# Kernel tuning notes

Hardware: AMD Instinct MI355X
Metric: run time of the kernel (lower is better)

## Reference

```python
import jax, jax.numpy as jnp
import numpy as np
import math

# hyperparams matching init_kwargs
GAMMA_S = 0.8
GAMMA_U = 0.8
RHO_I = 0.1
RHO_T = 0.1
EPS = 1e-10
TAU_MIN = 0.005
TAU_MAX = 1.0
TAU_INIT = 0.07
GRAD_CLIP = 5.0
ETA_INIT = 0.01
ETA_MIN = 0.0001
N_STATE = 2900000
BSZ = 4096
DIM = 1024


def setup_inputs() -> dict:
    key = jax.random.key(0)
    k1, k2 = jax.random.split(key)
    imf = jax.random.normal(k1, (BSZ, DIM), jnp.float32)
    imf = imf / jnp.linalg.norm(imf, axis=1, keepdims=True)
    txf = jax.random.normal(k2, (BSZ, DIM), jnp.float32)
    txf = txf / jnp.linalg.norm(txf, axis=1, keepdims=True)
    return {
        "image_features": imf,
        "text_features": txf,
        "s_I": jnp.zeros((N_STATE,), jnp.float32),
        "s_T": jnp.zeros((N_STATE,), jnp.float32),
        "tau_I": jnp.full((N_STATE,), TAU_INIT, jnp.float32),
        "tau_T": jnp.full((N_STATE,), TAU_INIT, jnp.float32),
        "u_I": jnp.zeros((N_STATE,), jnp.float32),
        "u_T": jnp.zeros((N_STATE,), jnp.float32),
        "b_I": jnp.zeros((N_STATE,), jnp.float32),
        "b_T": jnp.zeros((N_STATE,), jnp.float32),
        "image_ids": jnp.arange(BSZ, dtype=jnp.int32),
        "text_ids": jnp.arange(BSZ, dtype=jnp.int32),
        "epoch": 5,
        "max_epoch": 30,
    }


def reference(image_features, text_features, s_I, s_T, tau_I, tau_T,
              u_I, u_T, b_I, b_T, image_ids, text_ids, epoch, max_epoch):
    B = image_features.shape[0]
    sim = jnp.einsum('id,jd->ij', image_features, text_features)  # [B,B]
    diag_sim = jnp.diagonal(sim)                                  # [B]

    tau_image = tau_I[image_ids]  # [B]
    tau_text = tau_T[text_ids]    # [B]

    image_diffs = sim - diag_sim[:, None]
    text_diffs = sim - diag_sim[None, :]
    # .detach() in torch -> stop_gradient
    idt = jax.lax.stop_gradient(image_diffs / tau_image[:, None])
    tdt = jax.lax.stop_gradient(text_diffs / tau_text[None, :])

    # max-trick state b_I / b_T: running row/col max per sample id
    old_b_I = b_I[image_ids]
    new_b_I = jnp.maximum(jnp.max(idt, axis=1), old_b_I)  # [B]
    old_b_T = b_T[text_ids]
    new_b_T = jnp.maximum(jnp.max(tdt, axis=0), old_b_T)  # [B]

    exp_image_diffs = jnp.exp(idt - new_b_I[:, None])
    exp_text_diffs = jnp.exp(tdt - new_b_T[None, :])
    g_I = jnp.sum(exp_image_diffs, axis=1, keepdims=True) / (B - 1)  # [B,1]
    g_T = jnp.sum(exp_text_diffs, axis=0, keepdims=True) / (B - 1)   # [1,B]

    # moving-average s state (compute_last=False, last_g_* = None path)
    s_I_new = (1.0 - GAMMA_S) * s_I[image_ids] * jnp.exp(old_b_I - new_b_I) + GAMMA_S * g_I[:, 0]
    s_T_new = (1.0 - GAMMA_S) * s_T[text_ids] * jnp.exp(old_b_T - new_b_T) + GAMMA_S * g_T[0, :]
    s_I_b = s_I_new[:, None]  # same shape as g_I
    s_T_b = s_T_new[None, :]  # same shape as g_T

    weights_image = exp_image_diffs / (s_I_b + EPS)
    weights_text = exp_text_diffs / (s_T_b + EPS)

    image_loss = jnp.sum(weights_image * image_diffs, axis=1, keepdims=True) / (B - 1)
    text_loss = jnp.sum(weights_text * text_diffs, axis=0, keepdims=True) / (B - 1)
    total_loss = image_loss.mean() + text_loss.mean()

    grad_tau_image = (jnp.log(s_I_b) + new_b_I[:, None] + RHO_I
                      - jnp.sum(weights_image * idt, axis=1, keepdims=True) / (B - 1))
    grad_tau_text = (jnp.log(s_T_b) + new_b_T[None, :] + RHO_T
                     - jnp.sum(weights_text * tdt, axis=0, keepdims=True) / (B - 1))

    u_I_new = (1.0 - GAMMA_U) * u_I[image_ids] + GAMMA_U * jnp.clip(grad_tau_image[:, 0], -GRAD_CLIP, GRAD_CLIP)
    u_T_new = (1.0 - GAMMA_U) * u_T[text_ids] + GAMMA_U * jnp.clip(grad_tau_text[0, :], -GRAD_CLIP, GRAD_CLIP)

    eta_cur = ETA_MIN + (ETA_INIT - ETA_MIN) * math.cos(math.pi * (epoch / max_epoch) / 2)
    tau_I_new = jnp.clip(tau_image - eta_cur * u_I_new, TAU_MIN, TAU_MAX)
    tau_T_new = jnp.clip(tau_text - eta_cur * u_T_new, TAU_MIN, TAU_MAX)

    # scattered state writes (the module's in-place buffer updates)
    b_I_out = b_I.at[image_ids].set(new_b_I)
    b_T_out = b_T.at[text_ids].set(new_b_T)
    s_I_out = s_I.at[image_ids].set(s_I_new)
    s_T_out = s_T.at[text_ids].set(s_T_new)
    u_I_out = u_I.at[image_ids].set(u_I_new)
    u_T_out = u_T.at[text_ids].set(u_T_new)
    tau_I_out = tau_I.at[image_ids].set(tau_I_new)
    tau_T_out = tau_T.at[text_ids].set(tau_T_new)

    avg_image_tau = tau_image.mean()
    avg_text_tau = tau_text.mean()

    return (g_I, g_T, grad_tau_image, grad_tau_text, total_loss,
            avg_image_tau, avg_text_tau,
            s_I_out, s_T_out, u_I_out, u_T_out,
            b_I_out, b_T_out, tau_I_out, tau_T_out)
```

## Files before the change

### kernel.cpp

```cpp
#include <hip/hip_runtime.h>
#include <math.h>

#define BSZ 4096
#define DIM 1024
#define NST 2900000

constexpr float GAMMA_S   = 0.8f;
constexpr float GAMMA_U   = 0.8f;
constexpr float RHO_I_C   = 0.1f;
constexpr float RHO_T_C   = 0.1f;
constexpr float C_EPS     = 1e-10f;
constexpr float TAU_MIN_C = 0.005f;
constexpr float TAU_MAX_C = 1.0f;
constexpr float GCLIP     = 5.0f;
constexpr float ETA_INIT_C = 0.01f;
constexpr float ETA_MIN_C  = 1e-4f;
constexpr float PI_F       = 3.14159265358979323846f;

typedef __bf16 bf16x8 __attribute__((ext_vector_type(8)));
typedef float  f32x4  __attribute__((ext_vector_type(4)));

__device__ __forceinline__ unsigned short f2bf(float f) {
    unsigned int u = __float_as_uint(f);
    u += 0x7fffu + ((u >> 16) & 1u);
    return (unsigned short)(u >> 16);
}
__device__ __forceinline__ float bf2f(unsigned short s) {
    return __uint_as_float(((unsigned int)s) << 16);
}

__global__ __launch_bounds__(256) void conv_diag(const float* __restrict__ imf,
                                                 const float* __restrict__ txf,
                                                 unsigned short* __restrict__ abf,
                                                 unsigned short* __restrict__ bbf,
                                                 const float* __restrict__ tau_I,
                                                 const float* __restrict__ tau_T,
                                                 const float* __restrict__ b_I,
                                                 const float* __restrict__ b_T,
                                                 const int* __restrict__ iid,
                                                 const int* __restrict__ tid_,
                                                 float* diag, float* tauIg, float* tauTg,
                                                 float* obI, float* obT,
                                                 float* __restrict__ scal) {
    if (blockIdx.x == 0 && threadIdx.x < 3) scal[threadIdx.x] = 0.f;
    const int w  = threadIdx.x >> 6;
    const int ln = threadIdx.x & 63;
    const int i  = blockIdx.x * 4 + w;
    float dot = 0.f;
#pragma unroll
    for (int k = 0; k < 4; ++k) {
        const int off = i * DIM + k * 256 + ln * 4;
        float4 a = *(const float4*)&imf[off];
        float4 b = *(const float4*)&txf[off];
        ushort4 ra, rb;
        ra.x = f2bf(a.x); ra.y = f2bf(a.y); ra.z = f2bf(a.z); ra.w = f2bf(a.w);
        rb.x = f2bf(b.x); rb.y = f2bf(b.y); rb.z = f2bf(b.z); rb.w = f2bf(b.w);
        *(ushort4*)&abf[off] = ra;
        *(ushort4*)&bbf[off] = rb;
        dot += bf2f(ra.x) * bf2f(rb.x) + bf2f(ra.y) * bf2f(rb.y) +
               bf2f(ra.z) * bf2f(rb.z) + bf2f(ra.w) * bf2f(rb.w);
    }
#pragma unroll
    for (int m = 32; m; m >>= 1) dot += __shfl_xor(dot, m);
    if (ln == 0) {
        diag[i] = dot;
        const int id = iid[i];
        tauIg[i] = tau_I[id];
        obI[i]   = b_I[id];
        const int td = tid_[i];
        tauTg[i] = tau_T[td];
        obT[i]   = b_T[td];
    }
}

__device__ __forceinline__ void async16(const void* g, void* l) {
    __builtin_amdgcn_global_load_lds(
        (const __attribute__((address_space(1))) void*)g,
        (__attribute__((address_space(3))) void*)l, 16, 0, 0);
}

__global__ __launch_bounds__(256) void gemm_fused(const unsigned short* __restrict__ A,
                                                  const unsigned short* __restrict__ B,
                                                  const float* __restrict__ diag,
                                                  const float* __restrict__ tauIg,
                                                  const float* __restrict__ tauTg,
                                                  float* __restrict__ rpM,
                                                  float* __restrict__ rpE,
                                                  float* __restrict__ rpV,
                                                  float* __restrict__ cpM,
                                                  float* __restrict__ cpE,
                                                  float* __restrict__ cpV,
                                                  const float* __restrict__ s_I,
                                                  const float* __restrict__ s_T,
                                                  const float* __restrict__ u_I,
                                                  const float* __restrict__ u_T,
                                                  const float* __restrict__ b_I,
                                                  const float* __restrict__ b_T,
                                                  const float* __restrict__ tau_I,
                                                  const float* __restrict__ tau_T,
                                                  float* __restrict__ outbase) {
    __shared__ unsigned short As[128 * 64];
    __shared__ unsigned short Bs[128 * 64];

    const int tid = threadIdx.x;
    const int gid = ((blockIdx.x >> 4) << 3) | (blockIdx.x & 7);

    if ((blockIdx.x >> 3) & 1) {
        const size_t idx = (size_t)gid * 256 + tid;
        const size_t stride = (size_t)1024 * 256;
        const size_t NV = (NST - 1) / 4;
        const float* srcs[8] = {s_I, s_T, u_I, u_T, b_I, b_T, tau_I, tau_T};
#pragma unroll
        for (int a = 0; a < 8; ++a) {
            const float* s = srcs[a];
            float* d = outbase + (size_t)a * NST;
            for (size_t cidx = idx; cidx < NV; cidx += stride) {
                const float4 f = *(const float4*)&s[4 * cidx];
                const float nx = s[4 * cidx + 4];
                *(float4*)&d[1 + 4 * cidx] = make_float4(f.y, f.z, f.w, nx);
            }
            if (idx == 0) d[0] = s[0];
            if (idx < 3)  d[NST - 3 + idx] = s[NST - 3 + idx];
        }
        return;
    }

    const int bjIdx = gid & 31, biIdx = gid >> 5;
    const int bi = biIdx * 128;
    const int bj = bjIdx * 128;
    const int lane = tid & 63;
    const int wave = tid >> 6;
    const int m_base = (wave >> 1) * 64;
    const int n_base = (wave & 1) * 64;

    f32x4 acc[4][4];
#pragma unroll
    for (int m = 0; m < 4; ++m)
#pragma unroll
        for (int n = 0; n < 4; ++n)
            acc[m][n] = (f32x4){0.f, 0.f, 0.f, 0.f};

    const int mrow = lane & 15;
    const int q    = lane >> 4;

    for (int k0 = 0; k0 < DIM; k0 += 64) {
        __syncthreads();
#pragma unroll
        for (int j = 0; j < 4; ++j) {
            const int c   = tid + j * 256;
            const int row = c >> 3;
            const int kk  = ((c & 7) ^ (row & 7)) << 3;
            async16(&A[(size_t)(bi + row) * DIM + k0 + kk], &As[c * 8]);
            async16(&B[(size_t)(bj + row) * DIM + k0 + kk], &Bs[c * 8]);
        }
        __syncthreads();
#pragma unroll
        for (int ks = 0; ks < 2; ++ks) {
            bf16x8 af[4], bfr[4];
#pragma unroll
            for (int t = 0; t < 4; ++t) {
                const int rlA = m_base + t * 16 + mrow;
                const int rlB = n_base + t * 16 + mrow;
                const int slA = (((ks << 2) + q) ^ (rlA & 7)) << 3;
                const int slB = (((ks << 2) + q) ^ (rlB & 7)) << 3;
                af[t]  = *(const bf16x8*)&As[rlA * 64 + slA];
                bfr[t] = *(const bf16x8*)&Bs[rlB * 64 + slB];
            }
#pragma unroll
            for (int mt = 0; mt < 4; ++mt)
#pragma unroll
                for (int nt = 0; nt < 4; ++nt)
                    acc[mt][nt] = __builtin_amdgcn_mfma_f32_16x16x32_bf16(
                        af[mt], bfr[nt], acc[mt][nt], 0, 0, 0);
        }
    }

    __syncthreads();
    float* prm = (float*)Bs;
    if (tid < 128) {
        prm[tid]       = diag[bi + tid];
        prm[128 + tid] = 1.0f / tauIg[bi + tid];
        prm[256 + tid] = diag[bj + tid];
        prm[384 + tid] = 1.0f / tauTg[bj + tid];
    }
    __syncthreads();

    float* red = (float*)As;
    const int rowq = (lane >> 4) * 4;

#pragma unroll
    for (int mt = 0; mt < 4; ++mt)
#pragma unroll
        for (int r = 0; r < 4; ++r) {
            const int row_l = m_base + mt * 16 + rowq + r;
            const float dgr = prm[row_l];
            const float itr = prm[128 + row_l];
            float v0 = (acc[mt][0][r] - dgr) * itr;
            float v1 = (acc[mt][1][r] - dgr) * itr;
            float v2 = (acc[mt][2][r] - dgr) * itr;
            float v3 = (acc[mt][3][r] - dgr) * itr;
            float m = fmaxf(fmaxf(v0, v1), fmaxf(v2, v3));
#pragma unroll
            for (int x = 1; x <= 8; x <<= 1) m = fmaxf(m, __shfl_xor(m, x));
            const float e0 = __expf(v0 - m), e1 = __expf(v1 - m);
            const float e2 = __expf(v2 - m), e3 = __expf(v3 - m);
            float se = e0 + e1 + e2 + e3;
            float sv = e0 * v0 + e1 * v1 + e2 * v2 + e3 * v3;
#pragma unroll
            for (int x = 1; x <= 8; x <<= 1) {
                se += __shfl_xor(se, x);
                sv += __shfl_xor(sv, x);
            }
            if ((lane & 15) == 0) {
                const int idx = wave * 64 + mt * 16 + rowq + r;
                red[idx] = m; red[256 + idx] = se; red[512 + idx] = sv;
            }
        }

#pragma unroll
    for (int nt = 0; nt < 4; ++nt) {
        const int col_l = n_base + nt * 16 + (lane & 15);
        const float dgc = prm[256 + col_l];
        const float itc = prm[384 + col_l];
        float m = -INFINITY;
#pragma unroll
        for (int mt = 0; mt < 4; ++mt)
#pragma unroll
            for (int r = 0; r < 4; ++r)
                m = fmaxf(m, (acc[mt][nt][r] - dgc) * itc);
        m = fmaxf(m, __shfl_xor(m, 16));
        m = fmaxf(m, __shfl_xor(m, 32));
        float se = 0.f, sv = 0.f;
#pragma unroll
        for (int mt = 0; mt < 4; ++mt)
#pragma unroll
            for (int r = 0; r < 4; ++r) {
                const float v = (acc[mt][nt][r] - dgc) * itc;
                const float e = __expf(v - m);
                se += e; sv += e * v;
            }
        se += __shfl_xor(se, 16); se += __shfl_xor(se, 32);
        sv += __shfl_xor(sv, 16); sv += __shfl_xor(sv, 32);
        if (lane < 16) {
            const int idx = wave * 64 + nt * 16 + lane;
            red[768 + idx] = m; red[1024 + idx] = se; red[1280 + idx] = sv;
        }
    }
    __syncthreads();

    if (tid < 128) {
        const int rg = tid, li = rg & 63;
        const int w0 = (rg >> 6) * 2, w1 = w0 + 1;
        const float mA = red[w0 * 64 + li], mB = red[w1 * 64 + li];
        const float M = fmaxf(mA, mB);
        const float fA = __expf(mA - M), fB = __expf(mB - M);
        const size_t o = (size_t)bjIdx * BSZ + bi + rg;
        rpM[o] = M;
        rpE[o] = red[256 + w0 * 64 + li] * fA + red[256 + w1 * 64 + li] * fB;
        rpV[o] = red[512 + w0 * 64 + li] * fA + red[512 + w1 * 64 + li] * fB;
    } else {
        const int cg = tid - 128, li = cg & 63;
        const int w0 = cg >> 6, w1 = w0 + 2;
        const float mA = red[768 + w0 * 64 + li], mB = red[768 + w1 * 64 + li];
        const float M = fmaxf(mA, mB);
        const float fA = __expf(mA - M), fB = __expf(mB - M);
        const size_t o = (size_t)biIdx * BSZ + bj + cg;
        cpM[o] = M;
        cpE[o] = red[1024 + w0 * 64 + li] * fA + red[1024 + w1 * 64 + li] * fB;
        cpV[o] = red[1280 + w0 * 64 + li] * fA + red[1280 + w1 * 64 + li] * fB;
    }
}

__global__ __launch_bounds__(256) void finalize(const float* __restrict__ s_I,
                                                const float* __restrict__ s_T,
                                                const float* __restrict__ u_I,
                                                const float* __restrict__ u_T,
                                                const int* __restrict__ iid,
                                                const int* __restrict__ tid_,
                                                const int* __restrict__ epoch,
                                                const int* __restrict__ maxep,
                                                const float* __restrict__ tauIg,
                                                const float* __restrict__ tauTg,
                                                const float* __restrict__ obI,
                                                const float* __restrict__ obT,
                                                const float* __restrict__ rpM,
                                                const float* __restrict__ rpE,
                                                const float* __restrict__ rpV,
                                                const float* __restrict__ cpM,
                                                const float* __restrict__ cpE,
                                                const float* __restrict__ cpV,
                                                float* __restrict__ out) {
    const int side = blockIdx.x & 1;
    const int i0   = (blockIdx.x >> 1) * 64;
    const int w    = threadIdx.x >> 6;
    const int il   = threadIdx.x & 63;
    const int i    = i0 + il;

    const float* pM  = side ? cpM  : rpM;
    const float* pE  = side ? cpE  : rpE;
    const float* pV  = side ? cpV  : rpV;
    const float* tg  = side ? tauTg : tauIg;
    const float* obA = side ? obT  : obI;
    const float* sA  = side ? s_T  : s_I;
    const float* uA  = side ? u_T  : u_I;
    const int*   ids = side ? tid_ : iid;
    const float  rho = side ? RHO_T_C : RHO_I_C;

    float M[8], E[8], V[8];
#pragma unroll
    for (int k = 0; k < 8; ++k) {
        const size_t o = (size_t)(w * 8 + k) * BSZ + i;
        M[k] = pM[o]; E[k] = pE[o]; V[k] = pV[o];
    }
    float pm = M[0];
#pragma unroll
    for (int k = 1; k < 8; ++k) pm = fmaxf(pm, M[k]);

    __shared__ float lred[12][64];
    lred[w][il] = pm;
    __syncthreads();

    const float ob = obA[i];
    const float nb = fmaxf(fmaxf(fmaxf(lred[0][il], lred[1][il]),
                                 fmaxf(lred[2][il], lred[3][il])), ob);
    float se = 0.f, sv = 0.f;
#pragma unroll
    for (int k = 0; k < 8; ++k) {
        const float f = __expf(M[k] - nb);
        se += E[k] * f;
        sv += V[k] * f;
    }
    lred[4 + w][il] = se;
    lred[8 + w][il] = sv;
    __syncthreads();

    if (w == 0) {
        const float eta = ETA_MIN_C + (ETA_INIT_C - ETA_MIN_C) *
                          cosf(0.5f * PI_F * ((float)epoch[0] / (float)maxep[0]));
        const float invBm1 = 1.0f / (float)(BSZ - 1);
        const float invB   = 1.0f / (float)BSZ;

        const int   id  = ids[i];
        const float tau = tg[i];
        const float seT = (lred[4][il] + lred[5][il]) + (lred[6][il] + lred[7][il]);
        const float svT = (lred[8][il] + lred[9][il]) + (lred[10][il] + lred[11][il]);

        const float g     = seT * invBm1;
        const float s_new = (1.f - GAMMA_S) * sA[id] * __expf(ob - nb) + GAMMA_S * g;
        const float W     = svT * invBm1 / (s_new + C_EPS);
        const float grad  = logf(s_new) + nb + rho - W;
        const float gc    = fminf(fmaxf(grad, -GCLIP), GCLIP);
        const float u_new = (1.f - GAMMA_U) * uA[id] + GAMMA_U * gc;
        const float tau_new = fminf(fmaxf(tau - eta * u_new, TAU_MIN_C), TAU_MAX_C);

        float* o_g   = out + side * BSZ;
        float* o_gt  = out + (2 + side) * BSZ;
        float* stb   = out + 4 * BSZ + 3;
        float* o_s   = stb + (size_t)side * NST;
        float* o_u   = stb + (size_t)(2 + side) * NST;
        float* o_b   = stb + (size_t)(4 + side) * NST;
        float* o_t   = stb + (size_t)(6 + side) * NST;

        o_g[i]  = g;
        o_gt[i] = grad;
        o_s[id] = s_new;
        o_u[id] = u_new;
        o_b[id] = nb;
        o_t[id] = tau_new;

        float v0 = tau * W * invB;
        float v1 = tau * invB;
#pragma unroll
        for (int o2 = 32; o2; o2 >>= 1) {
            v0 += __shfl_down(v0, o2);
            v1 += __shfl_down(v1, o2);
        }
        if (il == 0) {
            atomicAdd(&out[4 * BSZ + 0], v0);
            atomicAdd(&out[4 * BSZ + 1 + side], v1);
        }
    }
}

extern "C" void kernel_launch(void* const* d_in, const int* in_sizes, int n_in,
                              void* d_out, int out_size, void* d_ws, size_t ws_size,
                              hipStream_t stream) {
    const float* imf   = (const float*)d_in[0];
    const float* txf   = (const float*)d_in[1];
    const float* s_I   = (const float*)d_in[2];
    const float* s_T   = (const float*)d_in[3];
    const float* tau_I = (const float*)d_in[4];
    const float* tau_T = (const float*)d_in[5];
    const float* u_I   = (const float*)d_in[6];
    const float* u_T   = (const float*)d_in[7];
    const float* b_I   = (const float*)d_in[8];
    const float* b_T   = (const float*)d_in[9];
    const int* iid     = (const int*)d_in[10];
    const int* tid_    = (const int*)d_in[11];
    const int* epoch   = (const int*)d_in[12];
    const int* maxep   = (const int*)d_in[13];

    float* out = (float*)d_out;
    float* ws  = (float*)d_ws;

    float* diag  = ws + 0 * BSZ;
    float* tauIg = ws + 1 * BSZ;
    float* tauTg = ws + 2 * BSZ;
    float* obI   = ws + 3 * BSZ;
    float* obT   = ws + 4 * BSZ;
    float* rpM   = ws + 5 * BSZ;
    float* rpE   = rpM + (size_t)32 * BSZ;
    float* rpV   = rpE + (size_t)32 * BSZ;
    float* cpM   = rpV + (size_t)32 * BSZ;
    float* cpE   = cpM + (size_t)32 * BSZ;
    float* cpV   = cpE + (size_t)32 * BSZ;
    unsigned short* abf = (unsigned short*)(cpV + (size_t)32 * BSZ);
    unsigned short* bbf = abf + (size_t)BSZ * DIM;

    conv_diag<<<BSZ / 4, 256, 0, stream>>>(imf, txf, abf, bbf, tau_I, tau_T, b_I, b_T,
                                           iid, tid_, diag, tauIg, tauTg, obI, obT,
                                           out + 4 * BSZ);
    gemm_fused<<<2048, 256, 0, stream>>>(abf, bbf, diag, tauIg, tauTg,
                                         rpM, rpE, rpV, cpM, cpE, cpV,
                                         s_I, s_T, u_I, u_T, b_I, b_T, tau_I, tau_T,
                                         out + 4 * BSZ + 3);
    finalize<<<128, 256, 0, stream>>>(s_I, s_T, u_I, u_T, iid, tid_, epoch, maxep,
                                      tauIg, tauTg, obI, obT,
                                      rpM, rpE, rpV, cpM, cpE, cpV, out);
}
```

Measured before the change: 305.4 us.

## Halve GEMM K-tile, remap block-to-tile order, shrink copy grid

```diff
diff --git a/kernel.cpp b/kernel.cpp
--- a/kernel.cpp
+++ b/kernel.cpp
@@ -99,15 +99,14 @@
                                                   const float* __restrict__ tau_I,
                                                   const float* __restrict__ tau_T,
                                                   float* __restrict__ outbase) {
-    __shared__ unsigned short As[128 * 64];
-    __shared__ unsigned short Bs[128 * 64];
+    __shared__ unsigned short As[128 * 32];
+    __shared__ unsigned short Bs[128 * 32];
 
     const int tid = threadIdx.x;
-    const int gid = ((blockIdx.x >> 4) << 3) | (blockIdx.x & 7);
-
-    if ((blockIdx.x >> 3) & 1) {
-        const size_t idx = (size_t)gid * 256 + tid;
-        const size_t stride = (size_t)1024 * 256;
+
+    if (blockIdx.x >= 1024) {
+        const size_t idx = (size_t)(blockIdx.x - 1024) * 256 + tid;
+        const size_t stride = (size_t)256 * 256;
         const size_t NV = (NST - 1) / 4;
         const float* srcs[8] = {s_I, s_T, u_I, u_T, b_I, b_T, tau_I, tau_T};
 #pragma unroll
@@ -115,9 +114,9 @@
             const float* s = srcs[a];
             float* d = outbase + (size_t)a * NST;
             for (size_t cidx = idx; cidx < NV; cidx += stride) {
-                const float4 f = *(const float4*)&s[4 * cidx];
-                const float nx = s[4 * cidx + 4];
-                *(float4*)&d[1 + 4 * cidx] = make_float4(f.y, f.z, f.w, nx);
+                const size_t e = 1 + 4 * cidx;
+                float4 v = make_float4(s[e], s[e + 1], s[e + 2], s[e + 3]);
+                *(float4*)&d[e] = v;
             }
             if (idx == 0) d[0] = s[0];
             if (idx < 3)  d[NST - 3 + idx] = s[NST - 3 + idx];
@@ -125,6 +124,7 @@
         return;
     }
 
+    const int gid = (blockIdx.x & 7) * 128 + (blockIdx.x >> 3);
     const int bjIdx = gid & 31, biIdx = gid >> 5;
     const int bi = biIdx * 128;
     const int bj = bjIdx * 128;
@@ -133,6 +133,10 @@
     const int m_base = (wave >> 1) * 64;
     const int n_base = (wave & 1) * 64;
 
+    const int c0 = tid, c1 = tid + 256;
+    const int r0 = c0 >> 2, kg0 = ((c0 & 3) ^ ((r0 >> 1) & 3)) * 8;
+    const int r1 = c1 >> 2, kg1 = ((c1 & 3) ^ ((r1 >> 1) & 3)) * 8;
+
     f32x4 acc[4][4];
 #pragma unroll
     for (int m = 0; m < 4; ++m)
@@ -143,36 +147,28 @@
     const int mrow = lane & 15;
     const int q    = lane >> 4;
 
-    for (int k0 = 0; k0 < DIM; k0 += 64) {
+    for (int k0 = 0; k0 < DIM; k0 += 32) {
         __syncthreads();
-#pragma unroll
-        for (int j = 0; j < 4; ++j) {
-            const int c   = tid + j * 256;
-            const int row = c >> 3;
-            const int kk  = ((c & 7) ^ (row & 7)) << 3;
-            async16(&A[(size_t)(bi + row) * DIM + k0 + kk], &As[c * 8]);
-            async16(&B[(size_t)(bj + row) * DIM + k0 + kk], &Bs[c * 8]);
-        }
+        async16(&A[(size_t)(bi + r0) * DIM + k0 + kg0], &As[c0 * 8]);
+        async16(&A[(size_t)(bi + r1) * DIM + k0 + kg1], &As[c1 * 8]);
+        async16(&B[(size_t)(bj + r0) * DIM + k0 + kg0], &Bs[c0 * 8]);
+        async16(&B[(size_t)(bj + r1) * DIM + k0 + kg1], &Bs[c1 * 8]);
         __syncthreads();
-#pragma unroll
-        for (int ks = 0; ks < 2; ++ks) {
-            bf16x8 af[4], bfr[4];
-#pragma unroll
-            for (int t = 0; t < 4; ++t) {
-                const int rlA = m_base + t * 16 + mrow;
-                const int rlB = n_base + t * 16 + mrow;
-                const int slA = (((ks << 2) + q) ^ (rlA & 7)) << 3;
-                const int slB = (((ks << 2) + q) ^ (rlB & 7)) << 3;
-                af[t]  = *(const bf16x8*)&As[rlA * 64 + slA];
-                bfr[t] = *(const bf16x8*)&Bs[rlB * 64 + slB];
-            }
-#pragma unroll
-            for (int mt = 0; mt < 4; ++mt)
-#pragma unroll
-                for (int nt = 0; nt < 4; ++nt)
-                    acc[mt][nt] = __builtin_amdgcn_mfma_f32_16x16x32_bf16(
-                        af[mt], bfr[nt], acc[mt][nt], 0, 0, 0);
-        }
+
+        bf16x8 af[4], bfr[4];
+#pragma unroll
+        for (int t = 0; t < 4; ++t) {
+            const int rlA = m_base + t * 16 + mrow;
+            const int rlB = n_base + t * 16 + mrow;
+            af[t]  = *(const bf16x8*)&As[rlA * 32 + (q ^ ((rlA >> 1) & 3)) * 8];
+            bfr[t] = *(const bf16x8*)&Bs[rlB * 32 + (q ^ ((rlB >> 1) & 3)) * 8];
+        }
+#pragma unroll
+        for (int mt = 0; mt < 4; ++mt)
+#pragma unroll
+            for (int nt = 0; nt < 4; ++nt)
+                acc[mt][nt] = __builtin_amdgcn_mfma_f32_16x16x32_bf16(
+                    af[mt], bfr[nt], acc[mt][nt], 0, 0, 0);
     }
 
     __syncthreads();
@@ -420,7 +416,7 @@
     conv_diag<<<BSZ / 4, 256, 0, stream>>>(imf, txf, abf, bbf, tau_I, tau_T, b_I, b_T,
                                            iid, tid_, diag, tauIg, tauTg, obI, obT,
                                            out + 4 * BSZ);
-    gemm_fused<<<2048, 256, 0, stream>>>(abf, bbf, diag, tauIg, tauTg,
+    gemm_fused<<<1280, 256, 0, stream>>>(abf, bbf, diag, tauIg, tauTg,
                                          rpM, rpE, rpV, cpM, cpE, cpV,
                                          s_I, s_T, u_I, u_T, b_I, b_T, tau_I, tau_T,
                                          out + 4 * BSZ + 3);
```

Measured after the change: 300.8 us. About the same (-1.5%).
